# Performance work log

Measured on AMD Instinct MI355X. Metric: run time of the kernel, lower is better.

The kernel has to match this reference:

```python
import jax, jax.numpy as jnp
import numpy as np

N, E, G = 25000, 400000, 64
IN, HID, OUT = 16, 16, 16
EF, EH, NH, NC = 8, 64, 128, 10
EPS = 1e-5


def _seg_mean(vals, idx, n):
    s = jax.ops.segment_sum(vals, idx, num_segments=n)
    c = jax.ops.segment_sum(jnp.ones((idx.shape[0], 1), vals.dtype), idx, num_segments=n)
    return s / jnp.maximum(c, 1.0)


def _bn(x, g, b):
    m = x.mean(axis=0)
    v = x.var(axis=0)
    return (x - m) * jax.lax.rsqrt(v + EPS) * g + b


def _nnconv(x, src, dst, ew, root, bias, n_nodes, out_ch):
    # ew: [E, in*out] -> per-edge weight matrix [E, in, out]
    ew = ew.reshape(ew.shape[0], x.shape[1], out_ch)
    msg = jnp.einsum('ei,eio->eo', x[src], ew)  # gather + per-edge matmul
    agg = _seg_mean(msg, dst, n_nodes)          # scatter-mean at target nodes
    return x @ root + agg + bias


def setup_inputs():
    key = jax.random.key(0)
    ks = jax.random.split(key, 24)
    f = lambda k, shp, sc: jax.random.normal(k, shp, dtype=jnp.float32) * sc
    inp = {
        'x': f(ks[0], (N, IN), 1.0),
        'edge_src': jax.random.randint(ks[1], (E,), 0, N, dtype=jnp.int32),
        'edge_dst': jax.random.randint(ks[2], (E,), 0, N, dtype=jnp.int32),
        'edge_attr': f(ks[3], (E, EF), 1.0),
        'batch': jnp.sort(jax.random.randint(ks[4], (N,), 0, G, dtype=jnp.int32)),
        # edge MLP 1: Linear(EF,EH) -> ReLU -> Linear(EH, IN*HID)
        'en1_w1': f(ks[5], (EF, EH), 0.3), 'en1_b1': jnp.zeros((EH,), jnp.float32),
        'en1_w2': f(ks[6], (EH, IN * HID), 0.1), 'en1_b2': jnp.zeros((IN * HID,), jnp.float32),
        'root1': f(ks[7], (IN, HID), 0.25), 'bias1': jnp.zeros((HID,), jnp.float32),
        'bn1_g': jnp.ones((HID,), jnp.float32), 'bn1_b': jnp.zeros((HID,), jnp.float32),
        # edge net 2 (FC): single Linear(EF, HID*OUT)
        'en2_w': f(ks[8], (EF, HID * OUT), 0.1), 'en2_b': jnp.zeros((HID * OUT,), jnp.float32),
        'root2': f(ks[9], (HID, OUT), 0.25), 'bias2': jnp.zeros((OUT,), jnp.float32),
        'bn2_g': jnp.ones((OUT,), jnp.float32), 'bn2_b': jnp.zeros((OUT,), jnp.float32),
        'mlp_w1': f(ks[10], (OUT, NH), 0.25), 'mlp_b1': jnp.zeros((NH,), jnp.float32),
        'mlp_w2': f(ks[11], (NH, NC), 0.1), 'mlp_b2': jnp.zeros((NC,), jnp.float32),
    }
    return inp


def reference(x, edge_src, edge_dst, edge_attr, batch,
              en1_w1, en1_b1, en1_w2, en1_b2, root1, bias1, bn1_g, bn1_b,
              en2_w, en2_b, root2, bias2, bn2_g, bn2_b,
              mlp_w1, mlp_b1, mlp_w2, mlp_b2):
    # NNConv layer 1 (edge MLP -> per-edge weight -> gather-matmul-scatter-mean)
    ew1 = jax.nn.relu(edge_attr @ en1_w1 + en1_b1) @ en1_w2 + en1_b2
    h = _nnconv(x, edge_src, edge_dst, ew1, root1, bias1, N, HID)
    h = _bn(h, bn1_g, bn1_b)
    # NNConv layer 2 (single-Linear edge net)
    ew2 = edge_attr @ en2_w + en2_b
    h = _nnconv(h, edge_src, edge_dst, ew2, root2, bias2, N, OUT)
    h = _bn(h, bn2_g, bn2_b)
    # graph-level mean pooling
    g = _seg_mean(h, batch, G)
    # MLP head + log_softmax
    logits = jax.nn.relu(g @ mlp_w1 + mlp_b1) @ mlp_w2 + mlp_b2
    return jax.nn.log_softmax(logits, axis=1)
```

## Files before the change

### kernel.cpp

```cpp
#include <hip/hip_runtime.h>

#define NN 25000
#define NE 400000
#define NGR 64
#define NB3 391
#define K1B 3125
#define HISTB 512
#define EPS 1e-5f

static const size_t OFS_XWBUF  = 0;
static const size_t OFS_H1     = 0;
static const size_t OFS_XB2    = 12800000;
static const size_t OFS_MSG    = 13200000;
static const size_t OFS_STATS  = 19600000;
static const size_t OFS_EREC   = 19625600;
static const size_t OFS_OFF    = 26025600;
static const size_t OFS_CSCOFF = 26051200;
static const size_t OFS_OUTC   = 26076800;
static const size_t OFS_INC    = 26102400;
static const size_t OFS_BSUM   = 26128000;
static const size_t OFS_PART1  = 26128512;
static const size_t OFS_PART2  = 26141024;

typedef __attribute__((ext_vector_type(8))) short v8s;
typedef __attribute__((ext_vector_type(4))) float v4f;

__device__ __forceinline__ void atomAddF(float* p, float v) { unsafeAtomicAdd(p, v); }

__device__ __forceinline__ float4 add4(float4 a, float4 b) {
  float4 r; r.x=a.x+b.x; r.y=a.y+b.y; r.z=a.z+b.z; r.w=a.w+b.w; return r;
}
__device__ __forceinline__ void fma4(float4& p, float r, const float4 a) {
  p.x += r*a.x; p.y += r*a.y; p.z += r*a.z; p.w += r*a.w;
}
__device__ __forceinline__ unsigned short f2bf(float f) {
  unsigned u = __float_as_uint(f);
  u += 0x7FFFu + ((u >> 16) & 1u);
  return (unsigned short)(u >> 16);
}

__global__ __launch_bounds__(256) void k_hist_xw(const int* __restrict__ esrc,
    const int* __restrict__ edst, int* __restrict__ outc, int* __restrict__ inc,
    const float* __restrict__ x, const float* __restrict__ w2, const float* __restrict__ b2,
    unsigned short* __restrict__ xwbuf, float* __restrict__ xb2) {
  __shared__ float xs[8][17];
  if (blockIdx.x >= K1B) {
    const int base = (blockIdx.x - K1B)*256 + threadIdx.x;
    for (int e = base; e < NE; e += HISTB*256) {
      atomicAdd(&outc[esrc[e]], 1);
      atomicAdd(&inc[edst[e]], 1);
    }
    return;
  }
  const int t = threadIdx.x;
  const int h = t >> 2;
  const int og = (t & 3) * 4;
  const int nbase = blockIdx.x * 8;
  if (t < 128) {
    const int n = nbase + (t >> 4), i = t & 15;
    xs[t >> 4][i] = (n < NN) ? x[(size_t)n*16 + i] : 0.f;
  }
  __syncthreads();
  float4 acc[8];
  #pragma unroll
  for (int n = 0; n < 8; ++n) acc[n] = make_float4(0.f,0.f,0.f,0.f);
  #pragma unroll
  for (int i = 0; i < 16; ++i) {
    const float4 w = *reinterpret_cast<const float4*>(&w2[h*256 + i*16 + og]);
    #pragma unroll
    for (int n = 0; n < 8; ++n) fma4(acc[n], xs[n][i], w);
  }
  #pragma unroll
  for (int n = 0; n < 8; ++n) {
    const int nn = nbase + n;
    if (nn < NN) {
      ushort4 s4;
      s4.x = f2bf(acc[n].x); s4.y = f2bf(acc[n].y);
      s4.z = f2bf(acc[n].z); s4.w = f2bf(acc[n].w);
      *reinterpret_cast<ushort4*>(&xwbuf[(size_t)nn*1024 + h*16 + og]) = s4;
    }
  }
  if (t < 128) {
    const int n = nbase + (t >> 4), o = t & 15;
    if (n < NN) {
      float s = 0.f;
      #pragma unroll
      for (int i = 0; i < 16; ++i) s += xs[t >> 4][i] * b2[i*16 + o];
      xb2[(size_t)n*16 + o] = s;
    }
  }
}

__global__ __launch_bounds__(256) void k0_scanA(const int* __restrict__ outc,
    const int* __restrict__ inc, int* __restrict__ bsum) {
  __shared__ int rO[256], rI[256];
  const int t = threadIdx.x;
  const int i = blockIdx.x*256 + t;
  rO[t] = outc[i];
  rI[t] = inc[i];
  __syncthreads();
  for (int st = 128; st > 0; st >>= 1) {
    if (t < st) { rO[t] += rO[t+st]; rI[t] += rI[t+st]; }
    __syncthreads();
  }
  if (t == 0) { bsum[blockIdx.x] = rO[0]; bsum[100 + blockIdx.x] = rI[0]; }
}

__global__ __launch_bounds__(128) void k0_scanB(int* __restrict__ bsum) {
  __shared__ int sO[128], sI[128];
  const int t = threadIdx.x;
  const int cO = (t < 100) ? bsum[t] : 0;
  const int cI = (t < 100) ? bsum[100 + t] : 0;
  sO[t] = cO; sI[t] = cI;
  __syncthreads();
  for (int st = 1; st < 128; st <<= 1) {
    const int vO = (t >= st) ? sO[t-st] : 0;
    const int vI = (t >= st) ? sI[t-st] : 0;
    __syncthreads();
    sO[t] += vO; sI[t] += vI;
    __syncthreads();
  }
  if (t < 100) { bsum[200 + t] = sO[t] - cO; bsum[300 + t] = sI[t] - cI; }
}

__global__ __launch_bounds__(256) void k0_scanC(int* __restrict__ outc,
    int* __restrict__ inc, const int* __restrict__ bsum,
    int* __restrict__ off, int* __restrict__ cscoff) {
  __shared__ int sO[256], sI[256];
  const int t = threadIdx.x;
  const int i = blockIdx.x*256 + t;
  const int cO = outc[i];
  const int cI = inc[i];
  sO[t] = cO; sI[t] = cI;
  __syncthreads();
  for (int st = 1; st < 256; st <<= 1) {
    const int vO = (t >= st) ? sO[t-st] : 0;
    const int vI = (t >= st) ? sI[t-st] : 0;
    __syncthreads();
    sO[t] += vO; sI[t] += vI;
    __syncthreads();
  }
  if (i <= NN) {
    off[i]    = sO[t] - cO + bsum[200 + blockIdx.x];
    cscoff[i] = sI[t] - cI + bsum[300 + blockIdx.x];
  }
  outc[i] = 0;
  inc[i]  = 0;
}

__global__ __launch_bounds__(256) void k0_fill(const int* __restrict__ esrc,
    const int* __restrict__ edst, const float* __restrict__ ea,
    int* __restrict__ curs, int* __restrict__ curd,
    const int* __restrict__ off, const int* __restrict__ cscoff,
    float* __restrict__ erec) {
  for (int e = blockIdx.x*blockDim.x + threadIdx.x; e < NE; e += gridDim.x*blockDim.x) {
    const int s = esrc[e], d = edst[e];
    const float4 a = *reinterpret_cast<const float4*>(&ea[(size_t)e*8]);
    const float4 b = *reinterpret_cast<const float4*>(&ea[(size_t)e*8 + 4]);
    const int c1 = atomicAdd(&curs[s], 1);
    const int c2 = atomicAdd(&curd[d], 1);
    float* r = &erec[(size_t)(off[s] + c1)*16];
    float4 c = make_float4(__int_as_float(cscoff[d] + c2), 0.f, 0.f, 0.f);
    float4 z = make_float4(0.f, 0.f, 0.f, 0.f);
    *reinterpret_cast<float4*>(r)      = a;
    *reinterpret_cast<float4*>(r + 4)  = b;
    *reinterpret_cast<float4*>(r + 8)  = c;
    *reinterpret_cast<float4*>(r + 12) = z;
  }
}

__global__ __launch_bounds__(256) void k2_csr(const float* __restrict__ erec,
    const float* __restrict__ w1, const float* __restrict__ b1,
    const unsigned short* __restrict__ xwbuf, const float* __restrict__ xb2,
    const int* __restrict__ off, float* __restrict__ msg) {
  __shared__ float w1s[512];
  __shared__ float b1s[64];
  for (int idx = threadIdx.x; idx < 512; idx += 256) w1s[idx] = w1[idx];
  if (threadIdx.x < 64) b1s[threadIdx.x] = b1[threadIdx.x];
  __syncthreads();
  const int lane = threadIdx.x & 63, wl = threadIdx.x >> 6;
  const int eidx = lane & 15;
  const int kg   = lane >> 4;
  const int hb0  = kg*8;
  const int hb1  = 32 + kg*8;
  const int gw = blockIdx.x*4 + wl, nw = gridDim.x*4;

  for (int n = gw; n < NN; n += nw) {
    const int st = off[n];
    const int deg = off[n+1] - st;
    if (deg == 0) continue;
    const unsigned short* xwn = &xwbuf[(size_t)n*1024];
    v8s bf0, bf1;
    #pragma unroll
    for (int j = 0; j < 8; ++j) {
      bf0[j] = (short)xwn[(hb0 + j)*16 + eidx];
      bf1[j] = (short)xwn[(hb1 + j)*16 + eidx];
    }
    const float xbv = xb2[(size_t)n*16 + eidx];

    for (int j0 = 0; j0 < deg; j0 += 16) {
      const int jj = j0 + eidx;
      const int slot = st + ((jj < deg) ? jj : (deg - 1));
      const float* rec = &erec[(size_t)slot*16];
      const float4 ea0 = *reinterpret_cast<const float4*>(rec);
      const float4 ea1 = *reinterpret_cast<const float4*>(rec + 4);
      const int pe = *reinterpret_cast<const int*>(rec + 8);
      const float eav[8] = {ea0.x, ea0.y, ea0.z, ea0.w, ea1.x, ea1.y, ea1.z, ea1.w};
      float4 rA0 = *reinterpret_cast<const float4*>(&b1s[hb0]);
      float4 rA1 = *reinterpret_cast<const float4*>(&b1s[hb0 + 4]);
      float4 rB0 = *reinterpret_cast<const float4*>(&b1s[hb1]);
      float4 rB1 = *reinterpret_cast<const float4*>(&b1s[hb1 + 4]);
      #pragma unroll
      for (int f = 0; f < 8; ++f) {
        const float ef = eav[f];
        fma4(rA0, ef, *reinterpret_cast<const float4*>(&w1s[f*64 + hb0]));
        fma4(rA1, ef, *reinterpret_cast<const float4*>(&w1s[f*64 + hb0 + 4]));
        fma4(rB0, ef, *reinterpret_cast<const float4*>(&w1s[f*64 + hb1]));
        fma4(rB1, ef, *reinterpret_cast<const float4*>(&w1s[f*64 + hb1 + 4]));
      }
      v8s af0, af1;
      af0[0] = (short)f2bf(fmaxf(rA0.x, 0.f)); af0[1] = (short)f2bf(fmaxf(rA0.y, 0.f));
      af0[2] = (short)f2bf(fmaxf(rA0.z, 0.f)); af0[3] = (short)f2bf(fmaxf(rA0.w, 0.f));
      af0[4] = (short)f2bf(fmaxf(rA1.x, 0.f)); af0[5] = (short)f2bf(fmaxf(rA1.y, 0.f));
      af0[6] = (short)f2bf(fmaxf(rA1.z, 0.f)); af0[7] = (short)f2bf(fmaxf(rA1.w, 0.f));
      af1[0] = (short)f2bf(fmaxf(rB0.x, 0.f)); af1[1] = (short)f2bf(fmaxf(rB0.y, 0.f));
      af1[2] = (short)f2bf(fmaxf(rB0.z, 0.f)); af1[3] = (short)f2bf(fmaxf(rB0.w, 0.f));
      af1[4] = (short)f2bf(fmaxf(rB1.x, 0.f)); af1[5] = (short)f2bf(fmaxf(rB1.y, 0.f));
      af1[6] = (short)f2bf(fmaxf(rB1.z, 0.f)); af1[7] = (short)f2bf(fmaxf(rB1.w, 0.f));

      v4f acc = {0.f, 0.f, 0.f, 0.f};
      acc = __builtin_amdgcn_mfma_f32_16x16x32_bf16(af0, bf0, acc, 0, 0, 0);
      acc = __builtin_amdgcn_mfma_f32_16x16x32_bf16(af1, bf1, acc, 0, 0, 0);

      #pragma unroll
      for (int r = 0; r < 4; ++r) {
        const int er = kg*4 + r;
        const int pr = __shfl(pe, er);
        if (j0 + er < deg)
          msg[(size_t)pr*16 + eidx] = acc[r] + xbv;
      }
    }
  }
}

__global__ __launch_bounds__(256) void k3_node1(const float* __restrict__ x,
    const float* __restrict__ root1, const float* __restrict__ bias1,
    const float* __restrict__ msg, const int* __restrict__ cscoff,
    const float* __restrict__ bn_g, const float* __restrict__ bn_b,
    float* __restrict__ h1, float* __restrict__ part,
    float* __restrict__ stats, int* __restrict__ cnt) {
  __shared__ float rt[256];
  __shared__ float red[2][64][16];
  __shared__ float fr[8][33];
  __shared__ int isLast;
  rt[threadIdx.x] = root1[threadIdx.x];
  const int nl = threadIdx.x >> 2, qd = threadIdx.x & 3;
  const int n = blockIdx.x*64 + nl;
  float4 s1 = {0,0,0,0}, s2 = {0,0,0,0};
  __syncthreads();
  if (n < NN) {
    const int b0 = cscoff[n];
    const int deg = cscoff[n+1] - b0;
    float4 sm = {0,0,0,0};
    for (int j = 0; j < deg; ++j)
      sm = add4(sm, *reinterpret_cast<const float4*>(&msg[(size_t)(b0+j)*16 + qd*4]));
    float4 acc = *reinterpret_cast<const float4*>(&bias1[qd*4]);
    #pragma unroll
    for (int i = 0; i < 16; ++i)
      fma4(acc, x[(size_t)n*16 + i], *reinterpret_cast<const float4*>(&rt[i*16 + qd*4]));
    const float inv = 1.f / (float)((deg > 0) ? deg : 1);
    fma4(acc, inv, sm);
    *reinterpret_cast<float4*>(&h1[(size_t)n*16 + qd*4]) = acc;
    s1 = acc;
    s2.x = acc.x*acc.x; s2.y = acc.y*acc.y; s2.z = acc.z*acc.z; s2.w = acc.w*acc.w;
  }
  *reinterpret_cast<float4*>(&red[0][nl][qd*4]) = s1;
  *reinterpret_cast<float4*>(&red[1][nl][qd*4]) = s2;
  __syncthreads();
  for (int st = 32; st > 0; st >>= 1) {
    if (nl < st) {
      #pragma unroll
      for (int k = 0; k < 4; ++k) {
        red[0][nl][qd*4+k] += red[0][nl+st][qd*4+k];
        red[1][nl][qd*4+k] += red[1][nl+st][qd*4+k];
      }
    }
    __syncthreads();
  }
  if (nl == 0) {
    *reinterpret_cast<float4*>(&part[blockIdx.x*32 + qd*4]) =
        *reinterpret_cast<const float4*>(&red[0][0][qd*4]);
    *reinterpret_cast<float4*>(&part[blockIdx.x*32 + 16 + qd*4]) =
        *reinterpret_cast<const float4*>(&red[1][0][qd*4]);
  }
  __syncthreads();
  if (threadIdx.x == 0) {
    __threadfence();
    isLast = (atomicAdd(cnt, 1) == NB3 - 1);
  }
  __syncthreads();
  if (!isLast) return;
  __threadfence();
  {
    const int o = threadIdx.x & 31, c = threadIdx.x >> 5;
    float s = 0.f;
    for (int blk = c; blk < NB3; blk += 8) s += part[blk*32 + o];
    fr[c][o] = s;
    __syncthreads();
    if (threadIdx.x < 32) {
      float tot = fr[0][threadIdx.x];
      for (int k = 1; k < 8; ++k) tot += fr[k][threadIdx.x];
      fr[0][threadIdx.x] = tot;
    }
    __syncthreads();
    if (threadIdx.x < 16) {
      const int oo = threadIdx.x;
      const float mean = fr[0][oo] / (float)NN;
      const float var  = fr[0][16+oo] / (float)NN - mean*mean;
      const float sc   = bn_g[oo] * rsqrtf(var + EPS);
      stats[32+oo] = sc;
      stats[48+oo] = bn_b[oo] - mean*sc;
    }
  }
}

__global__ __launch_bounds__(256) void k6_csr(const float* __restrict__ erec,
    const float* __restrict__ h1, const float* __restrict__ stats,
    const float* __restrict__ w, const float* __restrict__ bvec,
    const int* __restrict__ off, float* __restrict__ msg) {
  __shared__ float ws2[2048];
  __shared__ float bs2[256];
  __shared__ float hwS[4][128];
  __shared__ float hbS[4][32];
  for (int idx = threadIdx.x; idx < 2048; idx += 256) ws2[idx] = w[idx];
  bs2[threadIdx.x] = bvec[threadIdx.x];
  __syncthreads();
  const int lane = threadIdx.x & 63, wl = threadIdx.x >> 6;
  const int el = lane >> 2, q = lane & 3;
  const int f = lane >> 3, o2 = (lane & 7) * 2;
  const int gw = blockIdx.x*4 + wl, nw = gridDim.x*4;
  for (int n = gw; n < NN; n += nw) {
    const int st = off[n];
    const int deg = off[n+1] - st;
    if (deg == 0) continue;
    if (lane < 16)
      hbS[wl][lane] = h1[(size_t)n*16 + lane]*stats[32+lane] + stats[48+lane];
    __builtin_amdgcn_wave_barrier();
    float a0 = 0.f, a1 = 0.f;
    #pragma unroll
    for (int i = 0; i < 16; ++i) {
      const float hv = hbS[wl][i];
      a0 += hv * ws2[f*256 + i*16 + o2];
      a1 += hv * ws2[f*256 + i*16 + o2 + 1];
    }
    hwS[wl][f*16 + o2] = a0; hwS[wl][f*16 + o2 + 1] = a1;
    if (lane < 16) {
      float s = 0.f;
      #pragma unroll
      for (int i = 0; i < 16; ++i) s += hbS[wl][i] * bs2[i*16 + lane];
      hbS[wl][16 + lane] = s;
    }
    __builtin_amdgcn_wave_barrier();
    const float4 mb = *reinterpret_cast<const float4*>(&hbS[wl][16 + q*4]);
    for (int j0 = 0; j0 < deg; j0 += 16) {
      const int jj = j0 + el;
      const bool act = (jj < deg);
      const int slot = st + (act ? jj : 0);
      const float* rec = &erec[(size_t)slot*16];
      const float4 ea0 = *reinterpret_cast<const float4*>(rec);
      const float4 ea1 = *reinterpret_cast<const float4*>(rec + 4);
      const int pe = *reinterpret_cast<const int*>(rec + 8);
      const float ef[8] = {ea0.x, ea0.y, ea0.z, ea0.w, ea1.x, ea1.y, ea1.z, ea1.w};
      float4 m = mb;
      #pragma unroll
      for (int ff = 0; ff < 8; ++ff)
        fma4(m, ef[ff], *reinterpret_cast<const float4*>(&hwS[wl][ff*16 + q*4]));
      if (act)
        *reinterpret_cast<float4*>(&msg[(size_t)pe*16 + q*4]) = m;
    }
    __builtin_amdgcn_wave_barrier();
  }
}

__global__ __launch_bounds__(256) void k7_node2(const float* __restrict__ h1,
    const float* __restrict__ root2, const float* __restrict__ bias2,
    const float* __restrict__ msg, const int* __restrict__ cscoff,
    const int* __restrict__ batch, const float* __restrict__ bn_g,
    const float* __restrict__ bn_b, float* __restrict__ stats,
    float* __restrict__ part, int* __restrict__ cnt) {
  __shared__ float rt[256];
  __shared__ float scs[16], shs[16];
  __shared__ float red[2][64][16];
  __shared__ float pool[64*17];
  __shared__ float fr[8][33];
  __shared__ int isLast;
  rt[threadIdx.x] = root2[threadIdx.x];
  if (threadIdx.x < 16) { scs[threadIdx.x] = stats[32+threadIdx.x]; shs[threadIdx.x] = stats[48+threadIdx.x]; }
  for (int idx = threadIdx.x; idx < 64*17; idx += 256) pool[idx] = 0.f;
  const int nl = threadIdx.x >> 2, qd = threadIdx.x & 3;
  const int n = blockIdx.x*64 + nl;
  float4 s1 = {0,0,0,0}, s2 = {0,0,0,0};
  __syncthreads();
  if (n < NN) {
    const int b0 = cscoff[n];
    const int deg = cscoff[n+1] - b0;
    float4 sm = {0,0,0,0};
    for (int j = 0; j < deg; ++j)
      sm = add4(sm, *reinterpret_cast<const float4*>(&msg[(size_t)(b0+j)*16 + qd*4]));
    float4 acc = *reinterpret_cast<const float4*>(&bias2[qd*4]);
    #pragma unroll
    for (int i = 0; i < 16; ++i) {
      const float hbn = h1[(size_t)n*16 + i]*scs[i] + shs[i];
      fma4(acc, hbn, *reinterpret_cast<const float4*>(&rt[i*16 + qd*4]));
    }
    const float inv = 1.f / (float)((deg > 0) ? deg : 1);
    fma4(acc, inv, sm);
    s1 = acc;
    s2.x = acc.x*acc.x; s2.y = acc.y*acc.y; s2.z = acc.z*acc.z; s2.w = acc.w*acc.w;
    const int g = batch[n];
    atomicAdd(&pool[g*17 + qd*4 + 0], acc.x);
    atomicAdd(&pool[g*17 + qd*4 + 1], acc.y);
    atomicAdd(&pool[g*17 + qd*4 + 2], acc.z);
    atomicAdd(&pool[g*17 + qd*4 + 3], acc.w);
    if (qd == 0) atomicAdd(&pool[g*17 + 16], 1.0f);
  }
  *reinterpret_cast<float4*>(&red[0][nl][qd*4]) = s1;
  *reinterpret_cast<float4*>(&red[1][nl][qd*4]) = s2;
  __syncthreads();
  for (int st = 32; st > 0; st >>= 1) {
    if (nl < st) {
      #pragma unroll
      for (int k = 0; k < 4; ++k) {
        red[0][nl][qd*4+k] += red[0][nl+st][qd*4+k];
        red[1][nl][qd*4+k] += red[1][nl+st][qd*4+k];
      }
    }
    __syncthreads();
  }
  if (nl == 0) {
    *reinterpret_cast<float4*>(&part[blockIdx.x*32 + qd*4]) =
        *reinterpret_cast<const float4*>(&red[0][0][qd*4]);
    *reinterpret_cast<float4*>(&part[blockIdx.x*32 + 16 + qd*4]) =
        *reinterpret_cast<const float4*>(&red[1][0][qd*4]);
  }
  for (int idx = threadIdx.x; idx < 64*17; idx += 256) {
    const float v = pool[idx];
    if (v != 0.f) {
      const int g = idx / 17, c = idx - g*17;
      atomAddF((c < 16) ? &stats[128 + g*16 + c] : &stats[1152 + g], v);
    }
  }
  __syncthreads();
  if (threadIdx.x == 0) {
    __threadfence();
    isLast = (atomicAdd(cnt, 1) == NB3 - 1);
  }
  __syncthreads();
  if (!isLast) return;
  __threadfence();
  {
    const int o = threadIdx.x & 31, c = threadIdx.x >> 5;
    float s = 0.f;
    for (int blk = c; blk < NB3; blk += 8) s += part[blk*32 + o];
    fr[c][o] = s;
    __syncthreads();
    if (threadIdx.x < 32) {
      float tot = fr[0][threadIdx.x];
      for (int k = 1; k < 8; ++k) tot += fr[k][threadIdx.x];
      fr[0][threadIdx.x] = tot;
    }
    __syncthreads();
    if (threadIdx.x < 16) {
      const int oo = threadIdx.x;
      const float mean = fr[0][oo] / (float)NN;
      const float var  = fr[0][16+oo] / (float)NN - mean*mean;
      const float sc   = bn_g[oo] * rsqrtf(var + EPS);
      stats[96+oo]  = sc;
      stats[112+oo] = bn_b[oo] - mean*sc;
    }
  }
}

__global__ __launch_bounds__(128) void k10_head(const float* __restrict__ stats,
    const float* __restrict__ w1, const float* __restrict__ b1,
    const float* __restrict__ w2, const float* __restrict__ b2,
    float* __restrict__ out) {
  __shared__ float gm[16];
  __shared__ float a[128];
  __shared__ float l[10];
  __shared__ float mls[2];
  const int g = blockIdx.x, j = threadIdx.x;
  if (j < 16) {
    const float cnt = fmaxf(stats[1152 + g], 1.0f);
    gm[j] = (stats[128 + g*16 + j] / cnt) * stats[96 + j] + stats[112 + j];
  }
  __syncthreads();
  float s = b1[j];
  #pragma unroll
  for (int o = 0; o < 16; ++o) s += gm[o]*w1[o*128 + j];
  a[j] = fmaxf(s, 0.f);
  __syncthreads();
  if (j < 10) {
    float t = b2[j];
    #pragma unroll 16
    for (int k = 0; k < 128; ++k) t += a[k]*w2[k*10 + j];
    l[j] = t;
  }
  __syncthreads();
  if (j == 0) {
    float m = l[0];
    for (int c = 1; c < 10; ++c) m = fmaxf(m, l[c]);
    float se = 0.f;
    for (int c = 0; c < 10; ++c) se += expf(l[c]-m);
    mls[0] = m; mls[1] = logf(se);
  }
  __syncthreads();
  if (j < 10) out[g*10 + j] = l[j] - mls[0] - mls[1];
}

extern "C" void kernel_launch(void* const* d_in, const int* in_sizes, int n_in,
                              void* d_out, int out_size, void* d_ws, size_t ws_size,
                              hipStream_t stream) {
  const float* x      = (const float*)d_in[0];
  const int*   esrc   = (const int*)  d_in[1];
  const int*   edst   = (const int*)  d_in[2];
  const float* ea     = (const float*)d_in[3];
  const int*   batch  = (const int*)  d_in[4];
  const float* en1_w1 = (const float*)d_in[5];
  const float* en1_b1 = (const float*)d_in[6];
  const float* en1_w2 = (const float*)d_in[7];
  const float* en1_b2 = (const float*)d_in[8];
  const float* root1  = (const float*)d_in[9];
  const float* bias1  = (const float*)d_in[10];
  const float* bn1_g  = (const float*)d_in[11];
  const float* bn1_b  = (const float*)d_in[12];
  const float* en2_w  = (const float*)d_in[13];
  const float* en2_b  = (const float*)d_in[14];
  const float* root2  = (const float*)d_in[15];
  const float* bias2  = (const float*)d_in[16];
  const float* bn2_g  = (const float*)d_in[17];
  const float* bn2_b  = (const float*)d_in[18];
  const float* mlp_w1 = (const float*)d_in[19];
  const float* mlp_b1 = (const float*)d_in[20];
  const float* mlp_w2 = (const float*)d_in[21];
  const float* mlp_b2 = (const float*)d_in[22];
  float* out = (float*)d_out;
  float* ws  = (float*)d_ws;

  unsigned short* xwbuf = (unsigned short*)(ws + OFS_XWBUF);
  float* xb2    = ws + OFS_XB2;
  float* msg    = ws + OFS_MSG;
  float* stats  = ws + OFS_STATS;
  float* erec   = ws + OFS_EREC;
  float* h1     = ws + OFS_H1;
  float* part1  = ws + OFS_PART1;
  float* part2  = ws + OFS_PART2;
  int*   off    = (int*)(ws + OFS_OFF);
  int*   cscoff = (int*)(ws + OFS_CSCOFF);
  int*   outc   = (int*)(ws + OFS_OUTC);
  int*   inc    = (int*)(ws + OFS_INC);
  int*   bsum   = (int*)(ws + OFS_BSUM);
  int*   cnt1   = (int*)(stats + 1216);
  int*   cnt2   = (int*)(stats + 1217);

  hipMemsetAsync(outc,  0, 51200*sizeof(int), stream);
  hipMemsetAsync(stats, 0, 2048*sizeof(float), stream);

  hipLaunchKernelGGL(k_hist_xw, dim3(K1B + HISTB), dim3(256), 0, stream,
                     esrc, edst, outc, inc, x, en1_w2, en1_b2, xwbuf, xb2);
  hipLaunchKernelGGL(k0_scanA, dim3(100), dim3(256), 0, stream, outc, inc, bsum);
  hipLaunchKernelGGL(k0_scanB, dim3(1),   dim3(128), 0, stream, bsum);
  hipLaunchKernelGGL(k0_scanC, dim3(100), dim3(256), 0, stream, outc, inc, bsum, off, cscoff);
  hipLaunchKernelGGL(k0_fill,  dim3(1024),dim3(256), 0, stream, esrc, edst, ea, outc, inc,
                     off, cscoff, erec);

  hipLaunchKernelGGL(k2_csr,   dim3(1024), dim3(256), 0, stream, erec, en1_w1, en1_b1,
                     xwbuf, xb2, off, msg);
  hipLaunchKernelGGL(k3_node1, dim3(NB3),  dim3(256), 0, stream, x, root1, bias1, msg, cscoff,
                     bn1_g, bn1_b, h1, part1, stats, cnt1);

  hipLaunchKernelGGL(k6_csr,   dim3(1024), dim3(256), 0, stream, erec, h1, stats,
                     en2_w, en2_b, off, msg);
  hipLaunchKernelGGL(k7_node2, dim3(NB3),  dim3(256), 0, stream, h1, root2, bias2, msg, cscoff,
                     batch, bn2_g, bn2_b, stats, part2, cnt2);

  hipLaunchKernelGGL(k10_head, dim3(64), dim3(128), 0, stream, stats, mlp_w1, mlp_b1, mlp_w2, mlp_b2, out);
}
```

Before: 242.2 us.

## Record edge ranks during histogram using 8 partitioned counter arrays

The histogram kernel now spreads its atomic counters over 8 partitioned copies and records each edge's rank within its partition, so the fill pass no longer needs a second round of atomics. The scan kernels sum the partitions and write per-partition base offsets, and fill computes slots directly from stored ranks. This also splits the xw computation into its own kernel instead of merging it with the histogram. The cost is extra workspace traffic for the rank arrays and the 8x counter arrays, plus a larger memset.

New measurement: 225.3 us. 7.0% less time.

```diff
diff --git a/kernel.cpp b/kernel.cpp
--- a/kernel.cpp
+++ b/kernel.cpp
@@ -5,19 +5,23 @@
 #define NGR 64
 #define NB3 391
 #define K1B 3125
-#define HISTB 512
+#define NPAD 25600
 #define EPS 1e-5f
 
 static const size_t OFS_XWBUF  = 0;
 static const size_t OFS_H1     = 0;
 static const size_t OFS_XB2    = 12800000;
 static const size_t OFS_MSG    = 13200000;
+static const size_t OFS_RANKS  = 13200000;
+static const size_t OFS_RANKD  = 13600000;
+static const size_t OFS_OUTC8  = 14000000;
+static const size_t OFS_INC8   = 14204800;
+static const size_t OFS_BASE8  = 14409600;
+static const size_t OFS_CBASE8 = 14614400;
 static const size_t OFS_STATS  = 19600000;
 static const size_t OFS_EREC   = 19625600;
 static const size_t OFS_OFF    = 26025600;
 static const size_t OFS_CSCOFF = 26051200;
-static const size_t OFS_OUTC   = 26076800;
-static const size_t OFS_INC    = 26102400;
 static const size_t OFS_BSUM   = 26128000;
 static const size_t OFS_PART1  = 26128512;
 static const size_t OFS_PART2  = 26141024;
@@ -39,19 +43,10 @@
   return (unsigned short)(u >> 16);
 }
 
-__global__ __launch_bounds__(256) void k_hist_xw(const int* __restrict__ esrc,
-    const int* __restrict__ edst, int* __restrict__ outc, int* __restrict__ inc,
-    const float* __restrict__ x, const float* __restrict__ w2, const float* __restrict__ b2,
+__global__ __launch_bounds__(256) void k1_xw(const float* __restrict__ x,
+    const float* __restrict__ w2, const float* __restrict__ b2,
     unsigned short* __restrict__ xwbuf, float* __restrict__ xb2) {
   __shared__ float xs[8][17];
-  if (blockIdx.x >= K1B) {
-    const int base = (blockIdx.x - K1B)*256 + threadIdx.x;
-    for (int e = base; e < NE; e += HISTB*256) {
-      atomicAdd(&outc[esrc[e]], 1);
-      atomicAdd(&inc[edst[e]], 1);
-    }
-    return;
-  }
   const int t = threadIdx.x;
   const int h = t >> 2;
   const int og = (t & 3) * 4;
@@ -91,13 +86,29 @@
   }
 }
 
-__global__ __launch_bounds__(256) void k0_scanA(const int* __restrict__ outc,
-    const int* __restrict__ inc, int* __restrict__ bsum) {
+__global__ __launch_bounds__(256) void k0_hist(const int* __restrict__ esrc,
+    const int* __restrict__ edst, int* __restrict__ outc8, int* __restrict__ inc8,
+    int* __restrict__ rankS, int* __restrict__ rankD) {
+  const int p = blockIdx.x & 7;
+  int* oc = outc8 + p*NPAD;
+  int* ic = inc8  + p*NPAD;
+  for (int e = blockIdx.x*256 + threadIdx.x; e < NE; e += gridDim.x*256) {
+    const int c1 = atomicAdd(&oc[esrc[e]], 1);
+    const int c2 = atomicAdd(&ic[edst[e]], 1);
+    rankS[e] = (p << 28) | c1;
+    rankD[e] = (p << 28) | c2;
+  }
+}
+
+__global__ __launch_bounds__(256) void k0_scanA(const int* __restrict__ outc8,
+    const int* __restrict__ inc8, int* __restrict__ bsum) {
   __shared__ int rO[256], rI[256];
   const int t = threadIdx.x;
   const int i = blockIdx.x*256 + t;
-  rO[t] = outc[i];
-  rI[t] = inc[i];
+  int s = 0, si = 0;
+  #pragma unroll
+  for (int p = 0; p < 8; ++p) { s += outc8[p*NPAD + i]; si += inc8[p*NPAD + i]; }
+  rO[t] = s; rI[t] = si;
   __syncthreads();
   for (int st = 128; st > 0; st >>= 1) {
     if (t < st) { rO[t] += rO[t+st]; rI[t] += rI[t+st]; }
@@ -123,14 +134,20 @@
   if (t < 100) { bsum[200 + t] = sO[t] - cO; bsum[300 + t] = sI[t] - cI; }
 }
 
-__global__ __launch_bounds__(256) void k0_scanC(int* __restrict__ outc,
-    int* __restrict__ inc, const int* __restrict__ bsum,
-    int* __restrict__ off, int* __restrict__ cscoff) {
+__global__ __launch_bounds__(256) void k0_scanC(const int* __restrict__ outc8,
+    const int* __restrict__ inc8, const int* __restrict__ bsum,
+    int* __restrict__ off, int* __restrict__ cscoff,
+    int* __restrict__ base8, int* __restrict__ cbase8) {
   __shared__ int sO[256], sI[256];
   const int t = threadIdx.x;
   const int i = blockIdx.x*256 + t;
-  const int cO = outc[i];
-  const int cI = inc[i];
+  int co[8], ci[8];
+  int cO = 0, cI = 0;
+  #pragma unroll
+  for (int p = 0; p < 8; ++p) {
+    co[p] = outc8[p*NPAD + i]; cO += co[p];
+    ci[p] = inc8[p*NPAD + i];  cI += ci[p];
+  }
   sO[t] = cO; sI[t] = cI;
   __syncthreads();
   for (int st = 1; st < 256; st <<= 1) {
@@ -140,28 +157,32 @@
     sO[t] += vO; sI[t] += vI;
     __syncthreads();
   }
-  if (i <= NN) {
-    off[i]    = sO[t] - cO + bsum[200 + blockIdx.x];
-    cscoff[i] = sI[t] - cI + bsum[300 + blockIdx.x];
-  }
-  outc[i] = 0;
-  inc[i]  = 0;
+  const int offv = sO[t] - cO + bsum[200 + blockIdx.x];
+  const int cscv = sI[t] - cI + bsum[300 + blockIdx.x];
+  if (i <= NN) { off[i] = offv; cscoff[i] = cscv; }
+  int run = offv;
+  #pragma unroll
+  for (int p = 0; p < 8; ++p) { base8[p*NPAD + i] = run; run += co[p]; }
+  run = cscv;
+  #pragma unroll
+  for (int p = 0; p < 8; ++p) { cbase8[p*NPAD + i] = run; run += ci[p]; }
 }
 
 __global__ __launch_bounds__(256) void k0_fill(const int* __restrict__ esrc,
     const int* __restrict__ edst, const float* __restrict__ ea,
-    int* __restrict__ curs, int* __restrict__ curd,
-    const int* __restrict__ off, const int* __restrict__ cscoff,
+    const int* __restrict__ rankS, const int* __restrict__ rankD,
+    const int* __restrict__ base8, const int* __restrict__ cbase8,
     float* __restrict__ erec) {
   for (int e = blockIdx.x*blockDim.x + threadIdx.x; e < NE; e += gridDim.x*blockDim.x) {
     const int s = esrc[e], d = edst[e];
     const float4 a = *reinterpret_cast<const float4*>(&ea[(size_t)e*8]);
     const float4 b = *reinterpret_cast<const float4*>(&ea[(size_t)e*8 + 4]);
-    const int c1 = atomicAdd(&curs[s], 1);
-    const int c2 = atomicAdd(&curd[d], 1);
-    float* r = &erec[(size_t)(off[s] + c1)*16];
-    float4 c = make_float4(__int_as_float(cscoff[d] + c2), 0.f, 0.f, 0.f);
-    float4 z = make_float4(0.f, 0.f, 0.f, 0.f);
+    const int rs = rankS[e], rd = rankD[e];
+    const int slot = base8[(rs >> 28)*NPAD + s] + (rs & 0x0FFFFFFF);
+    const int pos  = cbase8[(rd >> 28)*NPAD + d] + (rd & 0x0FFFFFFF);
+    float* r = &erec[(size_t)slot*16];
+    const float4 c = make_float4(__int_as_float(pos), 0.f, 0.f, 0.f);
+    const float4 z = make_float4(0.f, 0.f, 0.f, 0.f);
     *reinterpret_cast<float4*>(r)      = a;
     *reinterpret_cast<float4*>(r + 4)  = b;
     *reinterpret_cast<float4*>(r + 8)  = c;
@@ -555,24 +576,30 @@
   float* h1     = ws + OFS_H1;
   float* part1  = ws + OFS_PART1;
   float* part2  = ws + OFS_PART2;
+  int*   rankS  = (int*)(ws + OFS_RANKS);
+  int*   rankD  = (int*)(ws + OFS_RANKD);
+  int*   outc8  = (int*)(ws + OFS_OUTC8);
+  int*   inc8   = (int*)(ws + OFS_INC8);
+  int*   base8  = (int*)(ws + OFS_BASE8);
+  int*   cbase8 = (int*)(ws + OFS_CBASE8);
   int*   off    = (int*)(ws + OFS_OFF);
   int*   cscoff = (int*)(ws + OFS_CSCOFF);
-  int*   outc   = (int*)(ws + OFS_OUTC);
-  int*   inc    = (int*)(ws + OFS_INC);
   int*   bsum   = (int*)(ws + OFS_BSUM);
   int*   cnt1   = (int*)(stats + 1216);
   int*   cnt2   = (int*)(stats + 1217);
 
-  hipMemsetAsync(outc,  0, 51200*sizeof(int), stream);
+  hipMemsetAsync(outc8, 0, 2*8*NPAD*sizeof(int), stream);
   hipMemsetAsync(stats, 0, 2048*sizeof(float), stream);
 
-  hipLaunchKernelGGL(k_hist_xw, dim3(K1B + HISTB), dim3(256), 0, stream,
-                     esrc, edst, outc, inc, x, en1_w2, en1_b2, xwbuf, xb2);
-  hipLaunchKernelGGL(k0_scanA, dim3(100), dim3(256), 0, stream, outc, inc, bsum);
-  hipLaunchKernelGGL(k0_scanB, dim3(1),   dim3(128), 0, stream, bsum);
-  hipLaunchKernelGGL(k0_scanC, dim3(100), dim3(256), 0, stream, outc, inc, bsum, off, cscoff);
-  hipLaunchKernelGGL(k0_fill,  dim3(1024),dim3(256), 0, stream, esrc, edst, ea, outc, inc,
-                     off, cscoff, erec);
+  hipLaunchKernelGGL(k1_xw, dim3(K1B), dim3(256), 0, stream, x, en1_w2, en1_b2, xwbuf, xb2);
+
+  hipLaunchKernelGGL(k0_hist,  dim3(1024), dim3(256), 0, stream, esrc, edst, outc8, inc8, rankS, rankD);
+  hipLaunchKernelGGL(k0_scanA, dim3(100),  dim3(256), 0, stream, outc8, inc8, bsum);
+  hipLaunchKernelGGL(k0_scanB, dim3(1),    dim3(128), 0, stream, bsum);
+  hipLaunchKernelGGL(k0_scanC, dim3(100),  dim3(256), 0, stream, outc8, inc8, bsum,
+                     off, cscoff, base8, cbase8);
+  hipLaunchKernelGGL(k0_fill,  dim3(1024), dim3(256), 0, stream, esrc, edst, ea,
+                     rankS, rankD, base8, cbase8, erec);
 
   hipLaunchKernelGGL(k2_csr,   dim3(1024), dim3(256), 0, stream, erec, en1_w1, en1_b1,
                      xwbuf, xb2, off, msg);
```
